# Kernel tuning notes

Hardware: AMD Instinct MI355X
Metric: run time of the kernel (lower is better)

## Reference

```python
import jax, jax.numpy as jnp
import numpy as np

XBITS = 8  # bitconfig['xbits']


def quantize(x, bits=XBITS):
    """Per-tensor dynamic fixed-point fake-quant.
    topk(|x|, k=len, largest=False).max() == max(|x|), so the 'percentile' is a no-op.
    scale = 2**(bits - ceil(log2(max|x|)) - 1); clamp(round(x*scale), -t, t)/scale.
    """
    thresh = float(2 ** (bits - 1) - 1)
    max_abs = jnp.max(jnp.abs(x))
    # get_scale returns 0 on log2 domain error (threshold <= 0)
    exp = jnp.where(max_abs > 0, jnp.ceil(jnp.log2(max_abs)), jnp.zeros((), x.dtype))
    scale = jnp.exp2(jnp.asarray(bits, x.dtype) - exp - 1)
    return jnp.clip(jnp.round(x * scale), -thresh, thresh) / scale


def setup_inputs() -> dict:
    key = jax.random.key(0)
    k1, k2, k3 = jax.random.split(key, 3)
    N, D_in, D_out = 65536, 1024, 1024
    x = jax.random.normal(k1, (N, D_in), dtype=jnp.float32)
    weight = jax.random.normal(k2, (D_out, D_in), dtype=jnp.float32) * (1.0 / np.sqrt(D_in))
    bias = jax.random.normal(k3, (D_out,), dtype=jnp.float32) * (1.0 / np.sqrt(D_in))
    return {"x": x, "weight": weight, "bias": bias}


def reference(x, weight, bias):
    # FixedLinearFunction.forward: quantize both operands, matmul; bias is NOT added.
    q_x = quantize(x)
    q_w = quantize(weight)
    return q_x @ q_w.T  # [N, D_out]
```

## Files before the change

kernel.cpp:

```cpp
#include <hip/hip_runtime.h>
#include <stdint.h>

typedef int v4i  __attribute__((ext_vector_type(4)));
typedef int v16i __attribute__((ext_vector_type(16)));

__device__ __forceinline__ void async_load16(const void* g, void* l) {
    auto gp = (const __attribute__((address_space(1))) unsigned int*)(uintptr_t)g;
    auto lp = (__attribute__((address_space(3))) unsigned int*)(unsigned int)(uintptr_t)l;
    __builtin_amdgcn_global_load_lds(gp, lp, 16, 0, 0);
}

__global__ void k_init(unsigned* bits) {
    if (threadIdx.x < 2) bits[threadIdx.x] = 0u;
}

__global__ void k_absmax(const float4* __restrict__ in, int n4,
                         unsigned* __restrict__ out_bits) {
    float m = 0.0f;
    int stride = gridDim.x * blockDim.x;
    for (int i = blockIdx.x * blockDim.x + threadIdx.x; i < n4; i += stride) {
        float4 v = in[i];
        m = fmaxf(m, fmaxf(fmaxf(fabsf(v.x), fabsf(v.y)),
                           fmaxf(fabsf(v.z), fabsf(v.w))));
    }
    #pragma unroll
    for (int off = 32; off > 0; off >>= 1)
        m = fmaxf(m, __shfl_down(m, off, 64));
    __shared__ float red[4];
    int lane = threadIdx.x & 63, wv = threadIdx.x >> 6;
    if (lane == 0) red[wv] = m;
    __syncthreads();
    if (threadIdx.x == 0) {
        m = fmaxf(fmaxf(red[0], red[1]), fmaxf(red[2], red[3]));
        atomicMax(out_bits, __float_as_uint(m));
    }
}

__global__ void k_scales(const unsigned* __restrict__ bits, float* __restrict__ sc) {
    float s[2];
    for (int i = 0; i < 2; ++i) {
        float m = __uint_as_float(bits[i]);
        int ex = 0;
        if (m > 0.0f) {
            int e;
            float f = frexpf(m, &e);
            ex = (f == 0.5f) ? (e - 1) : e;
        }
        s[i] = ldexpf(1.0f, 7 - ex);
    }
    sc[0] = s[0];
    sc[1] = s[1];
    sc[2] = 1.0f / (s[0] * s[1]);
}

__global__ void k_quant(const float4* __restrict__ in, int* __restrict__ out,
                        const float* __restrict__ scp, int n4) {
    float s = scp[0];
    int stride = gridDim.x * blockDim.x;
    for (int i = blockIdx.x * blockDim.x + threadIdx.x; i < n4; i += stride) {
        float4 v = in[i];
        int qa = (int)rintf(v.x * s); qa = qa > 127 ? 127 : (qa < -127 ? -127 : qa);
        int qb = (int)rintf(v.y * s); qb = qb > 127 ? 127 : (qb < -127 ? -127 : qb);
        int qc = (int)rintf(v.z * s); qc = qc > 127 ? 127 : (qc < -127 ? -127 : qc);
        int qd = (int)rintf(v.w * s); qd = qd > 127 ? 127 : (qd < -127 ? -127 : qd);
        out[i] = (qa & 0xff) | ((qb & 0xff) << 8) | ((qc & 0xff) << 16) | (qd << 24);
    }
}

__global__ __launch_bounds__(256) void k_gemm(const signed char* __restrict__ A,
                                              const signed char* __restrict__ B,
                                              float* __restrict__ out,
                                              const float* __restrict__ scp) {
    __shared__ __align__(16) signed char As[128 * 64];
    __shared__ __align__(16) signed char Bs[128 * 64];
    const int tid  = threadIdx.x;
    const int lane = tid & 63;
    const int wave = tid >> 6;
    const int wm   = wave & 1;
    const int wn   = wave >> 1;
    const int m0   = blockIdx.y * 128;
    const int n0   = blockIdx.x * 128;
    const int l31  = lane & 31;
    const int lhi  = lane >> 5;

    v16i acc[2][2];
    #pragma unroll
    for (int a = 0; a < 2; ++a)
        #pragma unroll
        for (int b = 0; b < 2; ++b)
            #pragma unroll
            for (int i = 0; i < 16; ++i) acc[a][b][i] = 0;

    const signed char* gA = A + (size_t)(m0 + (tid >> 2)) * 1024 + (tid & 3) * 16;
    const signed char* gB = B + (size_t)(n0 + (tid >> 2)) * 1024 + (tid & 3) * 16;
    signed char* lA = As + tid * 16;
    signed char* lB = Bs + tid * 16;

    for (int k0 = 0; k0 < 1024; k0 += 64) {
        async_load16(gA + k0,             lA);
        async_load16(gA + k0 + 64 * 1024, lA + 4096);
        async_load16(gB + k0,             lB);
        async_load16(gB + k0 + 64 * 1024, lB + 4096);
        __syncthreads();
        #pragma unroll
        for (int kc = 0; kc < 2; ++kc) {
            const int kb = kc * 32 + lhi * 16;
            v4i a0 = *(const v4i*)(As + (wm * 64 +      l31) * 64 + kb);
            v4i a1 = *(const v4i*)(As + (wm * 64 + 32 + l31) * 64 + kb);
            v4i b0 = *(const v4i*)(Bs + (wn * 64 +      l31) * 64 + kb);
            v4i b1 = *(const v4i*)(Bs + (wn * 64 + 32 + l31) * 64 + kb);
            acc[0][0] = __builtin_amdgcn_mfma_i32_32x32x32_i8(a0, b0, acc[0][0], 0, 0, 0);
            acc[0][1] = __builtin_amdgcn_mfma_i32_32x32x32_i8(a0, b1, acc[0][1], 0, 0, 0);
            acc[1][0] = __builtin_amdgcn_mfma_i32_32x32x32_i8(a1, b0, acc[1][0], 0, 0, 0);
            acc[1][1] = __builtin_amdgcn_mfma_i32_32x32x32_i8(a1, b1, acc[1][1], 0, 0, 0);
        }
        __syncthreads();
    }

    const float inv = scp[0];
    #pragma unroll
    for (int tm = 0; tm < 2; ++tm)
        #pragma unroll
        for (int tn = 0; tn < 2; ++tn)
            #pragma unroll
            for (int r = 0; r < 16; ++r) {
                int row = m0 + wm * 64 + tm * 32 + (r & 3) + 8 * (r >> 2) + 4 * lhi;
                int col = n0 + wn * 64 + tn * 32 + l31;
                out[(size_t)row * 1024 + col] = (float)acc[tm][tn][r] * inv;
            }
}

extern "C" void kernel_launch(void* const* d_in, const int* in_sizes, int n_in,
                              void* d_out, int out_size, void* d_ws, size_t ws_size,
                              hipStream_t stream) {
    const float* x = (const float*)d_in[0];
    const float* w = (const float*)d_in[1];
    float* out = (float*)d_out;

    const int NX = 65536 * 1024;
    const int NW = 1024 * 1024;

    char* ws = (char*)d_ws;
    unsigned* bits = (unsigned*)ws;
    float* sc = (float*)(ws + 8);
    signed char* qx = (signed char*)(ws + 256);
    signed char* qw = qx + (size_t)NX;

    k_init<<<1, 64, 0, stream>>>(bits);
    k_absmax<<<2048, 256, 0, stream>>>((const float4*)x, NX / 4, bits + 0);
    k_absmax<<<256, 256, 0, stream>>>((const float4*)w, NW / 4, bits + 1);
    k_scales<<<1, 1, 0, stream>>>(bits, sc);
    k_quant<<<4096, 256, 0, stream>>>((const float4*)x, (int*)qx, sc + 0, NX / 4);
    k_quant<<<512, 256, 0, stream>>>((const float4*)w, (int*)qw, sc + 1, NW / 4);

    dim3 grid(1024 / 128, 65536 / 128);
    k_gemm<<<grid, 256, 0, stream>>>(qx, qw, out, sc + 2);
}
```

Measured before the change: 602.5 us.

## Double-buffer GEMM LDS tiles and merge x/w absmax and quant launches

After: 658.7 us. +9.3%, slower.

```diff
diff --git a/kernel.cpp b/kernel.cpp
--- a/kernel.cpp
+++ b/kernel.cpp
@@ -14,15 +14,28 @@
     if (threadIdx.x < 2) bits[threadIdx.x] = 0u;
 }
 
-__global__ void k_absmax(const float4* __restrict__ in, int n4,
-                         unsigned* __restrict__ out_bits) {
-    float m = 0.0f;
-    int stride = gridDim.x * blockDim.x;
-    for (int i = blockIdx.x * blockDim.x + threadIdx.x; i < n4; i += stride) {
+__global__ void k_absmax(const float4* __restrict__ x, int n4x, int nbx,
+                         const float4* __restrict__ w, int n4w, int nbw,
+                         unsigned* __restrict__ bits) {
+    const float4* in;
+    int n4, b, nb;
+    unsigned* ob;
+    if ((int)blockIdx.x < nbx) { in = x; n4 = n4x; b = blockIdx.x; nb = nbx; ob = bits; }
+    else { in = w; n4 = n4w; b = blockIdx.x - nbx; nb = nbw; ob = bits + 1; }
+    float m0 = 0.f, m1 = 0.f;
+    int stride = nb * blockDim.x * 2;
+    for (int i = b * blockDim.x * 2 + threadIdx.x; i < n4; i += stride) {
         float4 v = in[i];
-        m = fmaxf(m, fmaxf(fmaxf(fabsf(v.x), fabsf(v.y)),
-                           fmaxf(fabsf(v.z), fabsf(v.w))));
+        m0 = fmaxf(m0, fmaxf(fmaxf(fabsf(v.x), fabsf(v.y)),
+                             fmaxf(fabsf(v.z), fabsf(v.w))));
+        int j = i + blockDim.x;
+        if (j < n4) {
+            float4 u = in[j];
+            m1 = fmaxf(m1, fmaxf(fmaxf(fabsf(u.x), fabsf(u.y)),
+                                 fmaxf(fabsf(u.z), fabsf(u.w))));
+        }
     }
+    float m = fmaxf(m0, m1);
     #pragma unroll
     for (int off = 32; off > 0; off >>= 1)
         m = fmaxf(m, __shfl_down(m, off, 64));
@@ -32,7 +45,7 @@
     __syncthreads();
     if (threadIdx.x == 0) {
         m = fmaxf(fmaxf(red[0], red[1]), fmaxf(red[2], red[3]));
-        atomicMax(out_bits, __float_as_uint(m));
+        atomicMax(ob, __float_as_uint(m));
     }
 }
 
@@ -48,16 +61,19 @@
         }
         s[i] = ldexpf(1.0f, 7 - ex);
     }
-    sc[0] = s[0];
-    sc[1] = s[1];
+    sc[0] = s[0]; sc[1] = s[1];
     sc[2] = 1.0f / (s[0] * s[1]);
 }
 
-__global__ void k_quant(const float4* __restrict__ in, int* __restrict__ out,
-                        const float* __restrict__ scp, int n4) {
-    float s = scp[0];
-    int stride = gridDim.x * blockDim.x;
-    for (int i = blockIdx.x * blockDim.x + threadIdx.x; i < n4; i += stride) {
+__global__ void k_quant(const float4* __restrict__ x, int* __restrict__ qx, int n4x, int nbx,
+                        const float4* __restrict__ w, int* __restrict__ qw, int n4w, int nbw,
+                        const float* __restrict__ scp) {
+    const float4* in; int* out;
+    int n4, b, nb; float s;
+    if ((int)blockIdx.x < nbx) { in = x; out = qx; n4 = n4x; b = blockIdx.x; nb = nbx; s = scp[0]; }
+    else { in = w; out = qw; n4 = n4w; b = blockIdx.x - nbx; nb = nbw; s = scp[1]; }
+    int stride = nb * blockDim.x;
+    for (int i = b * blockDim.x + threadIdx.x; i < n4; i += stride) {
         float4 v = in[i];
         int qa = (int)rintf(v.x * s); qa = qa > 127 ? 127 : (qa < -127 ? -127 : qa);
         int qb = (int)rintf(v.y * s); qb = qb > 127 ? 127 : (qb < -127 ? -127 : qb);
@@ -67,12 +83,11 @@
     }
 }
 
-__global__ __launch_bounds__(256) void k_gemm(const signed char* __restrict__ A,
-                                              const signed char* __restrict__ B,
-                                              float* __restrict__ out,
-                                              const float* __restrict__ scp) {
-    __shared__ __align__(16) signed char As[128 * 64];
-    __shared__ __align__(16) signed char Bs[128 * 64];
+__global__ __launch_bounds__(256, 3) void k_gemm(const signed char* __restrict__ A,
+                                                 const signed char* __restrict__ B,
+                                                 float* __restrict__ out,
+                                                 const float* __restrict__ scp) {
+    __shared__ __align__(16) signed char sm[2][2][8192];
     const int tid  = threadIdx.x;
     const int lane = tid & 63;
     const int wave = tid >> 6;
@@ -91,33 +106,44 @@
             #pragma unroll
             for (int i = 0; i < 16; ++i) acc[a][b][i] = 0;
 
-    const signed char* gA = A + (size_t)(m0 + (tid >> 2)) * 1024 + (tid & 3) * 16;
-    const signed char* gB = B + (size_t)(n0 + (tid >> 2)) * 1024 + (tid & 3) * 16;
-    signed char* lA = As + tid * 16;
-    signed char* lB = Bs + tid * 16;
+    const int L0 = tid, L1 = tid + 256;
+    const signed char* gA0 = A + (size_t)(m0 + (L0 & 127)) * 1024 + (L0 >> 7) * 16;
+    const signed char* gA1 = A + (size_t)(m0 + (L1 & 127)) * 1024 + (L1 >> 7) * 16;
+    const signed char* gB0 = B + (size_t)(n0 + (L0 & 127)) * 1024 + (L0 >> 7) * 16;
+    const signed char* gB1 = B + (size_t)(n0 + (L1 & 127)) * 1024 + (L1 >> 7) * 16;
 
-    for (int k0 = 0; k0 < 1024; k0 += 64) {
-        async_load16(gA + k0,             lA);
-        async_load16(gA + k0 + 64 * 1024, lA + 4096);
-        async_load16(gB + k0,             lB);
-        async_load16(gB + k0 + 64 * 1024, lB + 4096);
+    async_load16(gA0, &sm[0][0][L0 * 16]);
+    async_load16(gA1, &sm[0][0][L1 * 16]);
+    async_load16(gB0, &sm[0][1][L0 * 16]);
+    async_load16(gB1, &sm[0][1][L1 * 16]);
+
+    for (int it = 0; it < 16; ++it) {
         __syncthreads();
+        if (it < 15) {
+            const int k0 = (it + 1) * 64;
+            const int nb = (it + 1) & 1;
+            async_load16(gA0 + k0, &sm[nb][0][L0 * 16]);
+            async_load16(gA1 + k0, &sm[nb][0][L1 * 16]);
+            async_load16(gB0 + k0, &sm[nb][1][L0 * 16]);
+            async_load16(gB1 + k0, &sm[nb][1][L1 * 16]);
+        }
+        const signed char* As = sm[it & 1][0];
+        const signed char* Bs = sm[it & 1][1];
         #pragma unroll
         for (int kc = 0; kc < 2; ++kc) {
-            const int kb = kc * 32 + lhi * 16;
-            v4i a0 = *(const v4i*)(As + (wm * 64 +      l31) * 64 + kb);
-            v4i a1 = *(const v4i*)(As + (wm * 64 + 32 + l31) * 64 + kb);
-            v4i b0 = *(const v4i*)(Bs + (wn * 64 +      l31) * 64 + kb);
-            v4i b1 = *(const v4i*)(Bs + (wn * 64 + 32 + l31) * 64 + kb);
+            const int c = kc * 2 + lhi;
+            v4i a0 = *(const v4i*)(As + (c * 128 + wm * 64 +      l31) * 16);
+            v4i a1 = *(const v4i*)(As + (c * 128 + wm * 64 + 32 + l31) * 16);
+            v4i b0 = *(const v4i*)(Bs + (c * 128 + wn * 64 +      l31) * 16);
+            v4i b1 = *(const v4i*)(Bs + (c * 128 + wn * 64 + 32 + l31) * 16);
             acc[0][0] = __builtin_amdgcn_mfma_i32_32x32x32_i8(a0, b0, acc[0][0], 0, 0, 0);
             acc[0][1] = __builtin_amdgcn_mfma_i32_32x32x32_i8(a0, b1, acc[0][1], 0, 0, 0);
             acc[1][0] = __builtin_amdgcn_mfma_i32_32x32x32_i8(a1, b0, acc[1][0], 0, 0, 0);
             acc[1][1] = __builtin_amdgcn_mfma_i32_32x32x32_i8(a1, b1, acc[1][1], 0, 0, 0);
         }
-        __syncthreads();
     }
 
-    const float inv = scp[0];
+    const float inv = scp[2];
     #pragma unroll
     for (int tm = 0; tm < 2; ++tm)
         #pragma unroll
@@ -146,13 +172,17 @@
     signed char* qx = (signed char*)(ws + 256);
     signed char* qw = qx + (size_t)NX;
 
+    const int NBX_A = 8192, NBW_A = 128;
+    const int NBX_Q = 8192, NBW_Q = 128;
+
     k_init<<<1, 64, 0, stream>>>(bits);
-    k_absmax<<<2048, 256, 0, stream>>>((const float4*)x, NX / 4, bits + 0);
-    k_absmax<<<256, 256, 0, stream>>>((const float4*)w, NW / 4, bits + 1);
+    k_absmax<<<NBX_A + NBW_A, 256, 0, stream>>>(
+        (const float4*)x, NX / 4, NBX_A, (const float4*)w, NW / 4, NBW_A, bits);
     k_scales<<<1, 1, 0, stream>>>(bits, sc);
-    k_quant<<<4096, 256, 0, stream>>>((const float4*)x, (int*)qx, sc + 0, NX / 4);
-    k_quant<<<512, 256, 0, stream>>>((const float4*)w, (int*)qw, sc + 1, NW / 4);
+    k_quant<<<NBX_Q + NBW_Q, 256, 0, stream>>>(
+        (const float4*)x, (int*)qx, NX / 4, NBX_Q,
+        (const float4*)w, (int*)qw, NW / 4, NBW_Q, sc);
 
     dim3 grid(1024 / 128, 65536 / 128);
-    k_gemm<<<grid, 256, 0, stream>>>(qx, qw, out, sc + 2);
+    k_gemm<<<grid, 256, 0, stream>>>(qx, qw, out, sc);
 }
```
